# Kernel tuning notes

Hardware: AMD Instinct MI355X
Metric: run time of the kernel (lower is better)

The kernel has to match this reference:

```python
import jax, jax.numpy as jnp
import numpy as np

N_NODES = 100000
N_EDGES = 1600000
IN_DIM = 128
OUT_DIM = 128


def setup_inputs() -> dict:
    key = jax.random.key(0)
    k_x, k_r, k_c, k_v, k_w, k_b = jax.random.split(key, 6)
    x = jax.random.normal(k_x, (N_NODES, IN_DIM), dtype=jnp.float32)
    rows = jax.random.randint(k_r, (N_EDGES,), 0, N_NODES, dtype=jnp.int32)
    cols = jax.random.randint(k_c, (N_EDGES,), 0, N_NODES, dtype=jnp.int32)
    vals = jax.random.uniform(k_v, (N_EDGES,), dtype=jnp.float32)
    # nn.Linear(in_dim, out_dim): kaiming-uniform-ish init, exact values irrelevant
    bound = 1.0 / np.sqrt(IN_DIM)
    W = jax.random.uniform(k_w, (IN_DIM, OUT_DIM), dtype=jnp.float32, minval=-bound, maxval=bound)
    b = jax.random.uniform(k_b, (OUT_DIM,), dtype=jnp.float32, minval=-bound, maxval=bound)
    return {"x": x, "W": W, "b": b, "vals": vals, "rows": rows, "cols": cols}


def reference(x, W, b, vals, rows, cols):
    # x = self.linear(x)
    h = x @ W + b  # [N, out_dim]
    # x = torch.sparse.mm(adj, x): out[r] += vals[e] * h[cols[e]] for each edge e with rows[e]==r
    msgs = vals[:, None] * h[cols]  # [E, out_dim]
    out = jax.ops.segment_sum(msgs, rows, num_segments=N_NODES)  # [N, out_dim]
    return out
```

## Files before the change

### kernel.cpp

```cpp
#include <hip/hip_runtime.h>

#define N_NODES 100000
#define N_EDGES 1600000
#define DIM 128
#define NBKT 3125
#define B1   256
#define EPB  6250
#define CAP2 832
#define GEMM_NB 1563

typedef __attribute__((ext_vector_type(8))) short bf16x8;
typedef __attribute__((ext_vector_type(4))) float f32x4;

__device__ __forceinline__ unsigned short f2bf(float f) {
    unsigned u = __float_as_uint(f);
    u += 0x7FFF + ((u >> 16) & 1);
    return (unsigned short)(u >> 16);
}
__device__ __forceinline__ float bflo(unsigned u) { return __uint_as_float(u << 16); }
__device__ __forceinline__ float bfhi(unsigned u) { return __uint_as_float(u & 0xFFFF0000u); }

__global__ __launch_bounds__(256) void wt_pack(const float* __restrict__ W,
                                               uint4* __restrict__ wtf,
                                               int* __restrict__ gcnt) {
    const int t = blockIdx.x * 256 + threadIdx.x;
    for (int i = t; i < NBKT; i += 2048) gcnt[i] = 0;
    const int f = t >> 6;
    const int l = t & 63;
    const int kc = f >> 3, nt = f & 7;
    const int quad = l >> 4, n = l & 15;
    unsigned o[4];
    #pragma unroll
    for (int jj = 0; jj < 4; ++jj) {
        const int k0 = kc * 32 + quad * 8 + jj * 2;
        const unsigned short lo = f2bf(W[(k0 + 0) * DIM + nt * 16 + n]);
        const unsigned short hi = f2bf(W[(k0 + 1) * DIM + nt * 16 + n]);
        o[jj] = (unsigned)lo | ((unsigned)hi << 16);
    }
    wtf[t] = make_uint4(o[0], o[1], o[2], o[3]);
}

#define ROWSTRIDE 136
__global__ __launch_bounds__(256) void gemm_count(const float* __restrict__ x,
                                                  const uint4* __restrict__ wtf,
                                                  const float* __restrict__ b,
                                                  unsigned short* __restrict__ h,
                                                  const int* __restrict__ rows,
                                                  int* __restrict__ gcnt,
                                                  unsigned short* __restrict__ cnt16) {
    __shared__ uint4 smem4[4 * 16 * ROWSTRIDE / 8];
    if (blockIdx.x >= GEMM_NB) {
        int* c = (int*)smem4;
        const int k = blockIdx.x - GEMM_NB, t = threadIdx.x;
        for (int bb = t; bb < NBKT; bb += 256) c[bb] = 0;
        __syncthreads();
        const int e0 = k * EPB;
        #pragma unroll
        for (int i = 0; i < 6; ++i) {
            const int4 r4 = *(const int4*)&rows[e0 + (t + i * 256) * 4];
            atomicAdd(&c[r4.x >> 5], 1);
            atomicAdd(&c[r4.y >> 5], 1);
            atomicAdd(&c[r4.z >> 5], 1);
            atomicAdd(&c[r4.w >> 5], 1);
        }
        if (t < EPB - 6144) atomicAdd(&c[rows[e0 + 6144 + t] >> 5], 1);
        __syncthreads();
        for (int bb = t; bb < NBKT; bb += 256) {
            const int v = c[bb];
            cnt16[(size_t)k * NBKT + bb] = (unsigned short)v;
            if (v) atomicAdd(&gcnt[bb], v);
        }
        return;
    }

    const int wave = threadIdx.x >> 6;
    const int lane = threadIdx.x & 63;
    const int quad = lane >> 4;
    const int m = lane & 15;
    const int row_base = blockIdx.x * 64 + wave * 16;
    const int row = row_base + m;
    const bool rok = (row < N_NODES);

    uint4 bf[32];
    #pragma unroll
    for (int f = 0; f < 32; ++f) bf[f] = wtf[f * 64 + lane];

    bf16x8 af[4];
    #pragma unroll
    for (int kc = 0; kc < 4; ++kc) {
        float4 v0, v1;
        if (rok) {
            v0 = *(const float4*)&x[(size_t)row * DIM + kc * 32 + quad * 8];
            v1 = *(const float4*)&x[(size_t)row * DIM + kc * 32 + quad * 8 + 4];
        } else {
            v0 = make_float4(0.f, 0.f, 0.f, 0.f);
            v1 = make_float4(0.f, 0.f, 0.f, 0.f);
        }
        union { bf16x8 v; unsigned u[4]; } a;
        a.u[0] = (unsigned)f2bf(v0.x) | ((unsigned)f2bf(v0.y) << 16);
        a.u[1] = (unsigned)f2bf(v0.z) | ((unsigned)f2bf(v0.w) << 16);
        a.u[2] = (unsigned)f2bf(v1.x) | ((unsigned)f2bf(v1.y) << 16);
        a.u[3] = (unsigned)f2bf(v1.z) | ((unsigned)f2bf(v1.w) << 16);
        af[kc] = a.v;
    }

    f32x4 acc[8];
    #pragma unroll
    for (int nt = 0; nt < 8; ++nt) {
        const float bv = b[nt * 16 + m];
        acc[nt] = (f32x4){bv, bv, bv, bv};
    }

    #pragma unroll
    for (int kc = 0; kc < 4; ++kc) {
        #pragma unroll
        for (int nt = 0; nt < 8; ++nt) {
            union { uint4 u; bf16x8 v; } bb; bb.u = bf[kc * 8 + nt];
            acc[nt] = __builtin_amdgcn_mfma_f32_16x16x32_bf16(af[kc], bb.v, acc[nt], 0, 0, 0);
        }
    }

    unsigned short* sh = (unsigned short*)smem4 + wave * 16 * ROWSTRIDE;
    #pragma unroll
    for (int nt = 0; nt < 8; ++nt) {
        #pragma unroll
        for (int i = 0; i < 4; ++i)
            sh[(quad * 4 + i) * ROWSTRIDE + nt * 16 + m] = f2bf(acc[nt][i]);
    }
    __syncthreads();
    uint4* hv4 = (uint4*)h;
    const int seg = lane & 15;
    #pragma unroll
    for (int c = 0; c < 4; ++c) {
        const int rl = (lane >> 4) + c * 4;
        const int r = row_base + rl;
        const uint4 v = *(const uint4*)&sh[rl * ROWSTRIDE + seg * 8];
        if (r < N_NODES) hv4[(size_t)r * 16 + seg] = v;
    }
}

__global__ __launch_bounds__(1024) void p1_scan(const int* __restrict__ gcnt,
                                                int* __restrict__ bktbase,
                                                int* __restrict__ gcur) {
    __shared__ int s[1024];
    const int t = threadIdx.x;
    const int base = 4 * t;
    int x0 = (base + 0 < NBKT) ? gcnt[base + 0] : 0;
    int x1 = (base + 1 < NBKT) ? gcnt[base + 1] : 0;
    int x2 = (base + 2 < NBKT) ? gcnt[base + 2] : 0;
    int x3 = (base + 3 < NBKT) ? gcnt[base + 3] : 0;
    const int sum = x0 + x1 + x2 + x3;
    s[t] = sum;
    __syncthreads();
    for (int o = 1; o < 1024; o <<= 1) {
        const int add = (t >= o) ? s[t - o] : 0;
        __syncthreads();
        s[t] += add;
        __syncthreads();
    }
    int run = s[t] - sum;
    if (base + 0 < NBKT) { bktbase[base + 0] = run; gcur[base + 0] = run; run += x0; }
    if (base + 1 < NBKT) { bktbase[base + 1] = run; gcur[base + 1] = run; run += x1; }
    if (base + 2 < NBKT) { bktbase[base + 2] = run; gcur[base + 2] = run; run += x2; }
    if (base + 3 < NBKT) { bktbase[base + 3] = run; gcur[base + 3] = run; run += x3; }
    if (base <= NBKT && NBKT < base + 4) bktbase[NBKT] = run;
}

__global__ __launch_bounds__(256) void p1_scatter(const int* __restrict__ rows,
                                                  const int* __restrict__ cols,
                                                  const float* __restrict__ vals,
                                                  const unsigned short* __restrict__ cnt16,
                                                  int* __restrict__ gcur,
                                                  int2* __restrict__ binned) {
    __shared__ int cur[NBKT];
    const int k = blockIdx.x, t = threadIdx.x;
    for (int bb = t; bb < NBKT; bb += 256) {
        const int cc = cnt16[(size_t)k * NBKT + bb];
        if (cc) cur[bb] = atomicAdd(&gcur[bb], cc);
    }
    __syncthreads();
    const int e0 = k * EPB;
    #pragma unroll
    for (int i = 0; i < 6; ++i) {
        const int g = (t + i * 256) * 4;
        const int4   r4 = *(const int4*)&rows[e0 + g];
        const int4   c4 = *(const int4*)&cols[e0 + g];
        const float4 v4 = *(const float4*)&vals[e0 + g];
        int p;
        p = atomicAdd(&cur[r4.x >> 5], 1);
        binned[p] = make_int2(((r4.x & 31) << 24) | c4.x, __float_as_int(v4.x));
        p = atomicAdd(&cur[r4.y >> 5], 1);
        binned[p] = make_int2(((r4.y & 31) << 24) | c4.y, __float_as_int(v4.y));
        p = atomicAdd(&cur[r4.z >> 5], 1);
        binned[p] = make_int2(((r4.z & 31) << 24) | c4.z, __float_as_int(v4.z));
        p = atomicAdd(&cur[r4.w >> 5], 1);
        binned[p] = make_int2(((r4.w & 31) << 24) | c4.w, __float_as_int(v4.w));
    }
    if (t < EPB - 6144) {
        const int e = e0 + 6144 + t;
        const int r = rows[e];
        const int p = atomicAdd(&cur[r >> 5], 1);
        binned[p] = make_int2(((r & 31) << 24) | cols[e], __float_as_int(vals[e]));
    }
}

__global__ __launch_bounds__(128) void p2_gather(const unsigned* __restrict__ h32,
                                                 const int2* __restrict__ binned,
                                                 const int* __restrict__ bktbase,
                                                 float* __restrict__ out) {
    __shared__ int2 ebuf[CAP2];
    __shared__ int rcount[32], rstart[32], rcur[32];
    const int b = blockIdx.x, t = threadIdx.x;
    const int s0 = bktbase[b];
    const int n = bktbase[b + 1] - s0;

    int2 ereg[7];
    int nm = 0;
    #pragma unroll
    for (int jj = 0; jj < 7; ++jj) {
        const int j = t + jj * 128;
        if (j < n) { ereg[jj] = binned[s0 + j]; nm = jj + 1; }
    }

    if (t < 32) rcount[t] = 0;
    __syncthreads();
    #pragma unroll
    for (int jj = 0; jj < 7; ++jj)
        if (jj < nm) atomicAdd(&rcount[((unsigned)ereg[jj].x) >> 24], 1);
    __syncthreads();

    if (t < 64) {
        const int c = (t < 32) ? rcount[t] : 0;
        int v = c;
        #pragma unroll
        for (int o = 1; o < 32; o <<= 1) {
            const int u = __shfl_up(v, o, 64);
            if (t >= o) v += u;
        }
        if (t < 32) { rstart[t] = v - c; rcur[t] = v - c; }
    }
    __syncthreads();

    #pragma unroll
    for (int jj = 0; jj < 7; ++jj)
        if (jj < nm) {
            const int lr = ((unsigned)ereg[jj].x) >> 24;
            const int pos = atomicAdd(&rcur[lr], 1);
            ebuf[pos] = make_int2(ereg[jj].x & 0x00FFFFFF, ereg[jj].y);
        }
    __syncthreads();

    const int wave = t >> 6, lane = t & 63;
    const char* hbase = (const char*)h32;
    const unsigned lane4 = (unsigned)lane * 4u;

    for (int i = 0; i < 8; ++i) {
        const int lr0 = wave * 16 + i;
        const int lr1 = lr0 + 8;
        const int r0 = b * 32 + lr0;
        const int r1 = b * 32 + lr1;
        const int st0 = rstart[lr0], cn0 = rcount[lr0];
        const int st1 = rstart[lr1], cn1 = rcount[lr1];

        float a0x = 0.f, a0y = 0.f, c0x = 0.f, c0y = 0.f;
        float a1x = 0.f, a1y = 0.f, c1x = 0.f, c1y = 0.f;
        int j0 = 0, j1 = 0;

        while (j0 + 2 <= cn0 && j1 + 2 <= cn1) {
            const int2 e0 = ebuf[st0 + j0], e1 = ebuf[st0 + j0 + 1];
            const int2 f0 = ebuf[st1 + j1], f1 = ebuf[st1 + j1 + 1];
            const unsigned u0 = *(const unsigned*)(hbase + ((((unsigned)e0.x) << 8) | lane4));
            const unsigned u1 = *(const unsigned*)(hbase + ((((unsigned)e1.x) << 8) | lane4));
            const unsigned w0 = *(const unsigned*)(hbase + ((((unsigned)f0.x) << 8) | lane4));
            const unsigned w1 = *(const unsigned*)(hbase + ((((unsigned)f1.x) << 8) | lane4));
            const float v0 = __int_as_float(e0.y), v1 = __int_as_float(e1.y);
            const float s0v = __int_as_float(f0.y), s1v = __int_as_float(f1.y);
            a0x = fmaf(v0, bflo(u0), a0x);  a0y = fmaf(v0, bfhi(u0), a0y);
            c0x = fmaf(v1, bflo(u1), c0x);  c0y = fmaf(v1, bfhi(u1), c0y);
            a1x = fmaf(s0v, bflo(w0), a1x); a1y = fmaf(s0v, bfhi(w0), a1y);
            c1x = fmaf(s1v, bflo(w1), c1x); c1y = fmaf(s1v, bfhi(w1), c1y);
            j0 += 2; j1 += 2;
        }
        for (; j0 + 2 <= cn0; j0 += 2) {
            const int2 e0 = ebuf[st0 + j0], e1 = ebuf[st0 + j0 + 1];
            const unsigned u0 = *(const unsigned*)(hbase + ((((unsigned)e0.x) << 8) | lane4));
            const unsigned u1 = *(const unsigned*)(hbase + ((((unsigned)e1.x) << 8) | lane4));
            const float v0 = __int_as_float(e0.y), v1 = __int_as_float(e1.y);
            a0x = fmaf(v0, bflo(u0), a0x); a0y = fmaf(v0, bfhi(u0), a0y);
            c0x = fmaf(v1, bflo(u1), c0x); c0y = fmaf(v1, bfhi(u1), c0y);
        }
        if (j0 < cn0) {
            const int2 e0 = ebuf[st0 + j0];
            const unsigned u0 = *(const unsigned*)(hbase + ((((unsigned)e0.x) << 8) | lane4));
            const float v0 = __int_as_float(e0.y);
            a0x = fmaf(v0, bflo(u0), a0x); a0y = fmaf(v0, bfhi(u0), a0y);
        }
        for (; j1 + 2 <= cn1; j1 += 2) {
            const int2 f0 = ebuf[st1 + j1], f1 = ebuf[st1 + j1 + 1];
            const unsigned w0 = *(const unsigned*)(hbase + ((((unsigned)f0.x) << 8) | lane4));
            const unsigned w1 = *(const unsigned*)(hbase + ((((unsigned)f1.x) << 8) | lane4));
            const float s0v = __int_as_float(f0.y), s1v = __int_as_float(f1.y);
            a1x = fmaf(s0v, bflo(w0), a1x); a1y = fmaf(s0v, bfhi(w0), a1y);
            c1x = fmaf(s1v, bflo(w1), c1x); c1y = fmaf(s1v, bfhi(w1), c1y);
        }
        if (j1 < cn1) {
            const int2 f0 = ebuf[st1 + j1];
            const unsigned w0 = *(const unsigned*)(hbase + ((((unsigned)f0.x) << 8) | lane4));
            const float s0v = __int_as_float(f0.y);
            a1x = fmaf(s0v, bflo(w0), a1x); a1y = fmaf(s0v, bfhi(w0), a1y);
        }

        {
            float2 o; o.x = a0x + c0x; o.y = a0y + c0y;
            *(float2*)&out[(size_t)r0 * DIM + lane * 2] = o;
        }
        {
            float2 o; o.x = a1x + c1x; o.y = a1y + c1y;
            *(float2*)&out[(size_t)r1 * DIM + lane * 2] = o;
        }
    }
}

extern "C" void kernel_launch(void* const* d_in, const int* in_sizes, int n_in,
                              void* d_out, int out_size, void* d_ws, size_t ws_size,
                              hipStream_t stream) {
    const float* x    = (const float*)d_in[0];
    const float* W    = (const float*)d_in[1];
    const float* b    = (const float*)d_in[2];
    const float* vals = (const float*)d_in[3];
    const int*   rows = (const int*)d_in[4];
    const int*   cols = (const int*)d_in[5];
    float* out = (float*)d_out;

    char* ws = (char*)d_ws;
    unsigned short* h = (unsigned short*)(ws + 0);
    uint4* wtf    = (uint4*)(ws + 25600000);
    int*   gcnt   = (int*)  (ws + 25632768);
    int*   bktbase= (int*)  (ws + 25645280);
    int*   gcur   = (int*)  (ws + 25657792);
    unsigned short* cnt16 = (unsigned short*)(ws + 25670304);
    int2*  binned = (int2*) (ws + 27270304);

    wt_pack<<<8, 256, 0, stream>>>(W, wtf, gcnt);

    gemm_count<<<GEMM_NB + B1, 256, 0, stream>>>(x, wtf, b, h, rows, gcnt, cnt16);

    p1_scan<<<1, 1024, 0, stream>>>(gcnt, bktbase, gcur);

    p1_scatter<<<B1, 256, 0, stream>>>(rows, cols, vals, cnt16, gcur, binned);

    p2_gather<<<NBKT, 128, 0, stream>>>((const unsigned*)h, binned, bktbase, out);
}
```

Baseline: 242.4 us.

## Replace bucketed binning with per-row CSR counting and global-atomic scatter

Counts edges per destination row using global atomics, scans the 100k row counts in a single block, and scatters edges straight into row-sorted CSR order with global atomics. The gather kernel then loads a contiguous slice and reads row offsets directly, with no per-bucket local sort. This removes the per-block bucket histograms, the cnt16 array, and the shared-memory sort inside the gather. In exchange it relies on many contended global atomics, a serial single-block scan over 100k entries, and a CAPB cap that silently truncates buckets holding more than 704 edges.

```diff
diff --git a/kernel.cpp b/kernel.cpp
--- a/kernel.cpp
+++ b/kernel.cpp
@@ -3,11 +3,13 @@
 #define N_NODES 100000
 #define N_EDGES 1600000
 #define DIM 128
-#define NBKT 3125
-#define B1   256
-#define EPB  6250
-#define CAP2 832
 #define GEMM_NB 1563
+#define B1H  256
+#define EPBH 6250
+#define B1S  625
+#define EPBS 2560
+#define NB2  3125
+#define CAPB 704
 
 typedef __attribute__((ext_vector_type(8))) short bf16x8;
 typedef __attribute__((ext_vector_type(4))) float f32x4;
@@ -24,7 +26,7 @@
                                                uint4* __restrict__ wtf,
                                                int* __restrict__ gcnt) {
     const int t = blockIdx.x * 256 + threadIdx.x;
-    for (int i = t; i < NBKT; i += 2048) gcnt[i] = 0;
+    for (int i = t; i < N_NODES; i += 2048) gcnt[i] = 0;
     const int f = t >> 6;
     const int l = t & 63;
     const int kc = f >> 3, nt = f & 7;
@@ -46,30 +48,20 @@
                                                   const float* __restrict__ b,
                                                   unsigned short* __restrict__ h,
                                                   const int* __restrict__ rows,
-                                                  int* __restrict__ gcnt,
-                                                  unsigned short* __restrict__ cnt16) {
+                                                  int* __restrict__ gcnt) {
     __shared__ uint4 smem4[4 * 16 * ROWSTRIDE / 8];
     if (blockIdx.x >= GEMM_NB) {
-        int* c = (int*)smem4;
         const int k = blockIdx.x - GEMM_NB, t = threadIdx.x;
-        for (int bb = t; bb < NBKT; bb += 256) c[bb] = 0;
-        __syncthreads();
-        const int e0 = k * EPB;
+        const int e0 = k * EPBH;
         #pragma unroll
         for (int i = 0; i < 6; ++i) {
             const int4 r4 = *(const int4*)&rows[e0 + (t + i * 256) * 4];
-            atomicAdd(&c[r4.x >> 5], 1);
-            atomicAdd(&c[r4.y >> 5], 1);
-            atomicAdd(&c[r4.z >> 5], 1);
-            atomicAdd(&c[r4.w >> 5], 1);
-        }
-        if (t < EPB - 6144) atomicAdd(&c[rows[e0 + 6144 + t] >> 5], 1);
-        __syncthreads();
-        for (int bb = t; bb < NBKT; bb += 256) {
-            const int v = c[bb];
-            cnt16[(size_t)k * NBKT + bb] = (unsigned short)v;
-            if (v) atomicAdd(&gcnt[bb], v);
-        }
+            atomicAdd(&gcnt[r4.x], 1);
+            atomicAdd(&gcnt[r4.y], 1);
+            atomicAdd(&gcnt[r4.z], 1);
+            atomicAdd(&gcnt[r4.w], 1);
+        }
+        if (t < EPBH - 6144) atomicAdd(&gcnt[rows[e0 + 6144 + t]], 1);
         return;
     }
 
@@ -140,16 +132,14 @@
 }
 
 __global__ __launch_bounds__(1024) void p1_scan(const int* __restrict__ gcnt,
-                                                int* __restrict__ bktbase,
+                                                int* __restrict__ rowoff,
                                                 int* __restrict__ gcur) {
     __shared__ int s[1024];
     const int t = threadIdx.x;
-    const int base = 4 * t;
-    int x0 = (base + 0 < NBKT) ? gcnt[base + 0] : 0;
-    int x1 = (base + 1 < NBKT) ? gcnt[base + 1] : 0;
-    int x2 = (base + 2 < NBKT) ? gcnt[base + 2] : 0;
-    int x3 = (base + 3 < NBKT) ? gcnt[base + 3] : 0;
-    const int sum = x0 + x1 + x2 + x3;
+    const int lo = t * 98;
+    const int hi = (lo + 98 < N_NODES) ? lo + 98 : N_NODES;
+    int sum = 0;
+    for (int i = lo; i < hi; ++i) sum += gcnt[i];
     s[t] = sum;
     __syncthreads();
     for (int o = 1; o < 1024; o <<= 1) {
@@ -159,95 +149,58 @@
         __syncthreads();
     }
     int run = s[t] - sum;
-    if (base + 0 < NBKT) { bktbase[base + 0] = run; gcur[base + 0] = run; run += x0; }
-    if (base + 1 < NBKT) { bktbase[base + 1] = run; gcur[base + 1] = run; run += x1; }
-    if (base + 2 < NBKT) { bktbase[base + 2] = run; gcur[base + 2] = run; run += x2; }
-    if (base + 3 < NBKT) { bktbase[base + 3] = run; gcur[base + 3] = run; run += x3; }
-    if (base <= NBKT && NBKT < base + 4) bktbase[NBKT] = run;
+    for (int i = lo; i < hi; ++i) {
+        const int v = gcnt[i];
+        rowoff[i] = run; gcur[i] = run; run += v;
+    }
+    if (lo < N_NODES && hi == N_NODES) rowoff[N_NODES] = run;
 }
 
 __global__ __launch_bounds__(256) void p1_scatter(const int* __restrict__ rows,
                                                   const int* __restrict__ cols,
                                                   const float* __restrict__ vals,
-                                                  const unsigned short* __restrict__ cnt16,
                                                   int* __restrict__ gcur,
                                                   int2* __restrict__ binned) {
-    __shared__ int cur[NBKT];
     const int k = blockIdx.x, t = threadIdx.x;
-    for (int bb = t; bb < NBKT; bb += 256) {
-        const int cc = cnt16[(size_t)k * NBKT + bb];
-        if (cc) cur[bb] = atomicAdd(&gcur[bb], cc);
-    }
-    __syncthreads();
-    const int e0 = k * EPB;
-    #pragma unroll
-    for (int i = 0; i < 6; ++i) {
-        const int g = (t + i * 256) * 4;
-        const int4   r4 = *(const int4*)&rows[e0 + g];
-        const int4   c4 = *(const int4*)&cols[e0 + g];
-        const float4 v4 = *(const float4*)&vals[e0 + g];
+    const int e0 = k * EPBS;
+    #pragma unroll
+    for (int i = 0; i < 2; ++i) {
+        const int g = e0 + (t + i * 256) * 4;
+        const int4   r4 = *(const int4*)&rows[g];
+        const int4   c4 = *(const int4*)&cols[g];
+        const float4 v4 = *(const float4*)&vals[g];
         int p;
-        p = atomicAdd(&cur[r4.x >> 5], 1);
-        binned[p] = make_int2(((r4.x & 31) << 24) | c4.x, __float_as_int(v4.x));
-        p = atomicAdd(&cur[r4.y >> 5], 1);
-        binned[p] = make_int2(((r4.y & 31) << 24) | c4.y, __float_as_int(v4.y));
-        p = atomicAdd(&cur[r4.z >> 5], 1);
-        binned[p] = make_int2(((r4.z & 31) << 24) | c4.z, __float_as_int(v4.z));
-        p = atomicAdd(&cur[r4.w >> 5], 1);
-        binned[p] = make_int2(((r4.w & 31) << 24) | c4.w, __float_as_int(v4.w));
-    }
-    if (t < EPB - 6144) {
-        const int e = e0 + 6144 + t;
-        const int r = rows[e];
-        const int p = atomicAdd(&cur[r >> 5], 1);
-        binned[p] = make_int2(((r & 31) << 24) | cols[e], __float_as_int(vals[e]));
+        p = atomicAdd(&gcur[r4.x], 1); binned[p] = make_int2(c4.x, __float_as_int(v4.x));
+        p = atomicAdd(&gcur[r4.y], 1); binned[p] = make_int2(c4.y, __float_as_int(v4.y));
+        p = atomicAdd(&gcur[r4.z], 1); binned[p] = make_int2(c4.z, __float_as_int(v4.z));
+        p = atomicAdd(&gcur[r4.w], 1); binned[p] = make_int2(c4.w, __float_as_int(v4.w));
+    }
+    if (t < 128) {
+        const int g = e0 + 2048 + t * 4;
+        const int4   r4 = *(const int4*)&rows[g];
+        const int4   c4 = *(const int4*)&cols[g];
+        const float4 v4 = *(const float4*)&vals[g];
+        int p;
+        p = atomicAdd(&gcur[r4.x], 1); binned[p] = make_int2(c4.x, __float_as_int(v4.x));
+        p = atomicAdd(&gcur[r4.y], 1); binned[p] = make_int2(c4.y, __float_as_int(v4.y));
+        p = atomicAdd(&gcur[r4.z], 1); binned[p] = make_int2(c4.z, __float_as_int(v4.z));
+        p = atomicAdd(&gcur[r4.w], 1); binned[p] = make_int2(c4.w, __float_as_int(v4.w));
     }
 }
 
 __global__ __launch_bounds__(128) void p2_gather(const unsigned* __restrict__ h32,
                                                  const int2* __restrict__ binned,
-                                                 const int* __restrict__ bktbase,
+                                                 const int* __restrict__ rowoff,
                                                  float* __restrict__ out) {
-    __shared__ int2 ebuf[CAP2];
-    __shared__ int rcount[32], rstart[32], rcur[32];
+    __shared__ int2 ebuf[CAPB];
+    __shared__ int roff[33];
     const int b = blockIdx.x, t = threadIdx.x;
-    const int s0 = bktbase[b];
-    const int n = bktbase[b + 1] - s0;
-
-    int2 ereg[7];
-    int nm = 0;
-    #pragma unroll
-    for (int jj = 0; jj < 7; ++jj) {
-        const int j = t + jj * 128;
-        if (j < n) { ereg[jj] = binned[s0 + j]; nm = jj + 1; }
-    }
-
-    if (t < 32) rcount[t] = 0;
+    if (t < 33) roff[t] = rowoff[b * 32 + t];
     __syncthreads();
-    #pragma unroll
-    for (int jj = 0; jj < 7; ++jj)
-        if (jj < nm) atomicAdd(&rcount[((unsigned)ereg[jj].x) >> 24], 1);
-    __syncthreads();
-
-    if (t < 64) {
-        const int c = (t < 32) ? rcount[t] : 0;
-        int v = c;
-        #pragma unroll
-        for (int o = 1; o < 32; o <<= 1) {
-            const int u = __shfl_up(v, o, 64);
-            if (t >= o) v += u;
-        }
-        if (t < 32) { rstart[t] = v - c; rcur[t] = v - c; }
-    }
-    __syncthreads();
-
-    #pragma unroll
-    for (int jj = 0; jj < 7; ++jj)
-        if (jj < nm) {
-            const int lr = ((unsigned)ereg[jj].x) >> 24;
-            const int pos = atomicAdd(&rcur[lr], 1);
-            ebuf[pos] = make_int2(ereg[jj].x & 0x00FFFFFF, ereg[jj].y);
-        }
+    const int s0 = roff[0];
+    const int n0 = roff[32] - s0;
+    const int nn = (n0 < CAPB) ? n0 : CAPB;
+    for (int j = t; j < nn; j += 128) ebuf[j] = binned[s0 + j];
     __syncthreads();
 
     const int wave = t >> 6, lane = t & 63;
@@ -259,8 +212,8 @@
         const int lr1 = lr0 + 8;
         const int r0 = b * 32 + lr0;
         const int r1 = b * 32 + lr1;
-        const int st0 = rstart[lr0], cn0 = rcount[lr0];
-        const int st1 = rstart[lr1], cn1 = rcount[lr1];
+        const int st0 = roff[lr0] - s0, cn0 = roff[lr0 + 1] - roff[lr0];
+        const int st1 = roff[lr1] - s0, cn1 = roff[lr1 + 1] - roff[lr1];
 
         float a0x = 0.f, a0y = 0.f, c0x = 0.f, c0y = 0.f;
         float a1x = 0.f, a1y = 0.f, c1x = 0.f, c1y = 0.f;
@@ -336,18 +289,17 @@
     unsigned short* h = (unsigned short*)(ws + 0);
     uint4* wtf    = (uint4*)(ws + 25600000);
     int*   gcnt   = (int*)  (ws + 25632768);
-    int*   bktbase= (int*)  (ws + 25645280);
-    int*   gcur   = (int*)  (ws + 25657792);
-    unsigned short* cnt16 = (unsigned short*)(ws + 25670304);
-    int2*  binned = (int2*) (ws + 27270304);
+    int*   rowoff = (int*)  (ws + 26032768);
+    int*   gcur   = (int*)  (ws + 26432784);
+    int2*  binned = (int2*) (ws + 26832784);
 
     wt_pack<<<8, 256, 0, stream>>>(W, wtf, gcnt);
 
-    gemm_count<<<GEMM_NB + B1, 256, 0, stream>>>(x, wtf, b, h, rows, gcnt, cnt16);
-
-    p1_scan<<<1, 1024, 0, stream>>>(gcnt, bktbase, gcur);
-
-    p1_scatter<<<B1, 256, 0, stream>>>(rows, cols, vals, cnt16, gcur, binned);
-
-    p2_gather<<<NBKT, 128, 0, stream>>>((const unsigned*)h, binned, bktbase, out);
-}
+    gemm_count<<<GEMM_NB + B1H, 256, 0, stream>>>(x, wtf, b, h, rows, gcnt);
+
+    p1_scan<<<1, 1024, 0, stream>>>(gcnt, rowoff, gcur);
+
+    p1_scatter<<<B1S, 256, 0, stream>>>(rows, cols, vals, gcur, binned);
+
+    p2_gather<<<NB2, 128, 0, stream>>>((const unsigned*)h, binned, rowoff, out);
+}
```

After: 586.9 us. +142.1%, slower.
